# Optimization experiments

Measured on AMD Instinct MI355X. Metric: run time of the kernel, lower is better.

Reference implementation:

```python
import jax, jax.numpy as jnp
import numpy as np

EPS = 1e-12

def _l2norm(x):
    return x / jnp.maximum(jnp.linalg.norm(x, axis=-1, keepdims=True), EPS)

def setup_inputs() -> dict:
    key = jax.random.key(0)
    ks = jax.random.split(key, 11)
    B, L, HID, M = 64, 512, 768, 128
    R, P, T = 64, 8, 32
    return {
        "hidden_states": jax.random.normal(ks[0], (B, L, HID), dtype=jnp.float32),
        "ctx_mask": jax.random.randint(ks[1], (B, L), 0, 2, dtype=jnp.int32),
        "between_mask": jax.random.randint(ks[2], (B, L), 0, 2, dtype=jnp.int32),
        "subj_type_id": jax.random.randint(ks[3], (B,), 0, T, dtype=jnp.int32),
        "obj_type_id": jax.random.randint(ks[4], (B,), 0, T, dtype=jnp.int32),
        "subj_first": jax.random.randint(ks[5], (B,), 0, 2, dtype=jnp.int32),
        "proj_W": jax.random.normal(ks[6], (HID, M), dtype=jnp.float32) * 0.02,
        "label_probes": jax.random.normal(ks[7], (R, P, M), dtype=jnp.float32) * 0.02,
        "subj_type_W": jax.random.normal(ks[8], (T, M), dtype=jnp.float32) * 0.02,
        "obj_type_W": jax.random.normal(ks[9], (T, M), dtype=jnp.float32) * 0.02,
        "dir_W": jax.random.normal(ks[10], (2, M), dtype=jnp.float32) * 0.02,
    }

def reference(hidden_states, ctx_mask, between_mask, subj_type_id, obj_type_id,
              subj_first, proj_W, label_probes, subj_type_W, obj_type_W, dir_W):
    # Document token embeddings: project + L2 normalize. [B, L, M]
    D = _l2norm(hidden_states @ proj_W)

    between = between_mask.astype(bool)
    ctx = ctx_mask.astype(bool)
    has_between = jnp.any(between, axis=1)  # [B]
    evidence = jnp.where(has_between[:, None], between, ctx)  # [B, L]

    # Conditioned probes: [B, R, P, M]
    Q = (label_probes[None]
         + subj_type_W[subj_type_id][:, None, None]
         + obj_type_W[obj_type_id][:, None, None]
         + dir_W[subj_first][:, None, None])
    Q = _l2norm(Q)

    # MaxSim: [B, R, P, L]
    sim = jnp.einsum('brhm,blm->brhl', Q, D)
    sim = jnp.where(evidence[:, None, None, :], sim, -10000.0)
    mx = sim.max(axis=3)                        # [B, R, P]
    mx = jnp.where(mx > -1000.0, mx, 0.0)       # zero out fully-masked probes
    logits = mx.sum(axis=2)                     # [B, R]
    return logits
```

## Files before the change

### kernel.cpp

```cpp
#include <hip/hip_runtime.h>
#include <hip/hip_bf16.h>

typedef __attribute__((ext_vector_type(8))) __bf16 bf16x8;
typedef __attribute__((ext_vector_type(4))) float f32x4;

#define B_   64
#define L_   512
#define HID_ 768
#define M_   128
#define R_   64
#define P_   8

__device__ __forceinline__ int swz(int row, int k, int stride) {
    return row * stride + (k ^ ((row & 7) << 3));
}
__device__ __forceinline__ int swz4(int row, int k) {
    return row * 128 + (k ^ ((row & 15) << 3));
}

#define GLL16(gp, lp)                                                        \
    __builtin_amdgcn_global_load_lds(                                        \
        (const __attribute__((address_space(1))) void*)(gp),                 \
        (__attribute__((address_space(3))) void*)(lp), 16, 0, 0)

__device__ __forceinline__ bf16x8 cvt8(float4 f0, float4 f1) {
    bf16x8 v;
    v[0]=(__bf16)f0.x; v[1]=(__bf16)f0.y; v[2]=(__bf16)f0.z; v[3]=(__bf16)f0.w;
    v[4]=(__bf16)f1.x; v[5]=(__bf16)f1.y; v[6]=(__bf16)f1.z; v[7]=(__bf16)f1.w;
    return v;
}

__global__ __launch_bounds__(256) void k_wt(const float* __restrict__ W,
                                            __bf16* __restrict__ Wt) {
    int idx = blockIdx.x * 256 + threadIdx.x;
    int k = idx >> 7, n = idx & 127;
    int c = k >> 6, kk = k & 63;
    Wt[c * 8192 + n * 64 + (kk ^ ((n & 7) << 3))] = (__bf16)W[idx];
}

__global__ __launch_bounds__(512, 4) void k_proj(const float* __restrict__ hidden,
                                                 const __bf16* __restrict__ Wt,
                                                 __bf16* __restrict__ D) {
    __shared__ __align__(16) __bf16 Al[2][64 * 64];
    __shared__ __align__(16) __bf16 Bl[2][128 * 64];
    __shared__ float nbuf[2][64];
    const int t = threadIdx.x;
    const int lane = t & 63, w = t >> 6;
    const int rlo = lane & 15, g = lane >> 4;
    const int rb = w & 3, ch = w >> 2;
    const int row0 = blockIdx.x * 512 + blockIdx.y * 64;

    f32x4 acc[4] = {};

    const int ar = t >> 3;
    const int ac = (t & 7) * 8;
    const float* arow = hidden + (size_t)(row0 + ar) * HID_ + ac;

    GLL16(Wt + w * 1024 + lane * 8,       &Bl[0][w * 1024]);
    GLL16(Wt + w * 1024 + 512 + lane * 8, &Bl[0][w * 1024 + 512]);
    {
        float4 f0 = *(const float4*)(arow);
        float4 f1 = *(const float4*)(arow + 4);
        *(bf16x8*)&Al[0][swz(ar, ac, 64)] = cvt8(f0, f1);
    }
    __syncthreads();

    for (int ci = 0; ci < 12; ++ci) {
        const int cur = ci & 1;
        const bool pre = ci < 11;
        float4 f0, f1;
        if (pre) {
            const __bf16* wsrc = Wt + (ci + 1) * 8192 + w * 1024;
            GLL16(wsrc + lane * 8,       &Bl[cur ^ 1][w * 1024]);
            GLL16(wsrc + 512 + lane * 8, &Bl[cur ^ 1][w * 1024 + 512]);
            const float* src = arow + (ci + 1) * 64;
            f0 = *(const float4*)(src);
            f1 = *(const float4*)(src + 4);
        }
#pragma unroll
        for (int s = 0; s < 2; ++s) {
            int kk = s * 32 + g * 8;
            bf16x8 aF = *(const bf16x8*)&Al[cur][swz(rb * 16 + rlo, kk, 64)];
#pragma unroll
            for (int c = 0; c < 4; ++c) {
                bf16x8 bF = *(const bf16x8*)&Bl[cur][swz(ch * 64 + c * 16 + rlo, kk, 64)];
                acc[c] = __builtin_amdgcn_mfma_f32_16x16x32_bf16(aF, bF, acc[c], 0, 0, 0);
            }
        }
        if (pre) {
            *(bf16x8*)&Al[cur ^ 1][swz(ar, ac, 64)] = cvt8(f0, f1);
        }
        __syncthreads();
    }

    float ss[4] = {0.f, 0.f, 0.f, 0.f};
#pragma unroll
    for (int c = 0; c < 4; ++c)
#pragma unroll
        for (int r = 0; r < 4; ++r) ss[r] += acc[c][r] * acc[c][r];
#pragma unroll
    for (int r = 0; r < 4; ++r)
#pragma unroll
        for (int off = 1; off < 16; off <<= 1) ss[r] += __shfl_xor(ss[r], off);
    if (rlo == 0) {
#pragma unroll
        for (int r = 0; r < 4; ++r) nbuf[ch][rb * 16 + g * 4 + r] = ss[r];
    }
    __syncthreads();
    float sc[4];
#pragma unroll
    for (int r = 0; r < 4; ++r) {
        float tot = nbuf[0][rb * 16 + g * 4 + r] + nbuf[1][rb * 16 + g * 4 + r];
        sc[r] = 1.0f / fmaxf(sqrtf(tot), 1e-12f);
    }

    __bf16* Dst = (__bf16*)Al;
#pragma unroll
    for (int c = 0; c < 4; ++c)
#pragma unroll
        for (int r = 0; r < 4; ++r) {
            int row = rb * 16 + g * 4 + r;
            int col = ch * 64 + c * 16 + rlo;
            Dst[swz4(row, col)] = (__bf16)(acc[c][r] * sc[r]);
        }
    __syncthreads();
#pragma unroll
    for (int h = 0; h < 2; ++h) {
        int row = (t >> 4) + h * 32;
        int seg = t & 15;
        bf16x8 v = *(const bf16x8*)&Dst[row * 128 + seg * 8];
        *(bf16x8*)(D + (size_t)(row0 + row) * M_ + seg * 8) = v;
    }
}

__global__ __launch_bounds__(256) void k_sim(const float* __restrict__ lp,
                                             const float* __restrict__ sW,
                                             const float* __restrict__ oW,
                                             const float* __restrict__ dW,
                                             const int* __restrict__ st,
                                             const int* __restrict__ ot,
                                             const int* __restrict__ sf,
                                             const int* __restrict__ ctx,
                                             const int* __restrict__ btw,
                                             const __bf16* __restrict__ D,
                                             float* __restrict__ out) {
    __shared__ __align__(16) __bf16 Dl[2][128 * 128];
    __shared__ float evl[L_];
    __shared__ int anyf;
    const int t = threadIdx.x;
    const int lane = t & 63, w = t >> 6;
    const int rlo = lane & 15, g = lane >> 4;
    const int b = blockIdx.x, pt = blockIdx.y;

    const __bf16* Db = D + (size_t)b * L_ * M_;

#pragma unroll
    for (int q = 0; q < 8; ++q)
        GLL16(Db + q * 2048 + w * 512 + lane * 8, &Dl[0][q * 2048 + w * 512]);

    if (t == 0) anyf = 0;
    __syncthreads();
    int v0 = btw[b * L_ + t], v1 = btw[b * L_ + t + 256];
    int c0 = ctx[b * L_ + t], c1 = ctx[b * L_ + t + 256];
    if (v0 | v1) anyf = 1;
    __syncthreads();
    const int any = anyf;
    evl[t]       = (any ? v0 : c0) ? 1.0f : 0.0f;
    evl[t + 256] = (any ? v1 : c1) ? 1.0f : 0.0f;

    const int sb = st[b], ob = ot[b], db = sf[b];
    const float* sv = sW + sb * M_;
    const float* ov = oW + ob * M_;
    const float* dv = dW + db * M_;
    bf16x8 qF[2][4];
#pragma unroll
    for (int pt2 = 0; pt2 < 2; ++pt2) {
        const float* lpp = lp + (size_t)(pt * 128 + w * 32 + pt2 * 16 + rlo) * M_;
        float qv[32];
        float ssq = 0.f;
#pragma unroll
        for (int ks = 0; ks < 4; ++ks) {
#pragma unroll
            for (int h = 0; h < 2; ++h) {
                const int m0 = ks * 32 + g * 8 + h * 4;
                float4 a  = *(const float4*)(lpp + m0);
                float4 s4 = *(const float4*)(sv + m0);
                float4 o4 = *(const float4*)(ov + m0);
                float4 d4 = *(const float4*)(dv + m0);
                float x0 = a.x + s4.x + o4.x + d4.x;
                float x1 = a.y + s4.y + o4.y + d4.y;
                float x2 = a.z + s4.z + o4.z + d4.z;
                float x3 = a.w + s4.w + o4.w + d4.w;
                qv[ks * 8 + h * 4 + 0] = x0;
                qv[ks * 8 + h * 4 + 1] = x1;
                qv[ks * 8 + h * 4 + 2] = x2;
                qv[ks * 8 + h * 4 + 3] = x3;
                ssq += x0 * x0 + x1 * x1 + x2 * x2 + x3 * x3;
            }
        }
        ssq += __shfl_xor(ssq, 16);
        ssq += __shfl_xor(ssq, 32);
        const float scq = 1.0f / fmaxf(sqrtf(ssq), 1e-12f);
#pragma unroll
        for (int ks = 0; ks < 4; ++ks)
#pragma unroll
            for (int j = 0; j < 8; ++j)
                qF[pt2][ks][j] = (__bf16)(qv[ks * 8 + j] * scq);
    }

    __syncthreads();

    float vmax[2][4];
#pragma unroll
    for (int pt2 = 0; pt2 < 2; ++pt2)
#pragma unroll
        for (int r = 0; r < 4; ++r) vmax[pt2][r] = -1e30f;

    for (int tc = 0; tc < 4; ++tc) {
        const int cur = tc & 1;
        if (tc < 3) {
#pragma unroll
            for (int q = 0; q < 8; ++q)
                GLL16(Db + (tc + 1) * 16384 + q * 2048 + w * 512 + lane * 8,
                      &Dl[cur ^ 1][q * 2048 + w * 512]);
        }
#pragma unroll
        for (int tt = 0; tt < 8; ++tt) {
            f32x4 pacc[2] = {};
#pragma unroll
            for (int ks = 0; ks < 4; ++ks) {
                bf16x8 bF = *(const bf16x8*)&Dl[cur][swz4(tt * 16 + rlo, ks * 32 + g * 8)];
                pacc[0] = __builtin_amdgcn_mfma_f32_16x16x32_bf16(qF[0][ks], bF, pacc[0], 0, 0, 0);
                pacc[1] = __builtin_amdgcn_mfma_f32_16x16x32_bf16(qF[1][ks], bF, pacc[1], 0, 0, 0);
            }
            const float e = evl[tc * 128 + tt * 16 + rlo];
#pragma unroll
            for (int pt2 = 0; pt2 < 2; ++pt2)
#pragma unroll
                for (int r = 0; r < 4; ++r) {
                    float sv2 = (e > 0.5f) ? pacc[pt2][r] : -1e4f;
                    vmax[pt2][r] = fmaxf(vmax[pt2][r], sv2);
                }
        }
        __syncthreads();
    }

#pragma unroll
    for (int pt2 = 0; pt2 < 2; ++pt2)
#pragma unroll
        for (int r = 0; r < 4; ++r)
#pragma unroll
            for (int off = 1; off < 16; off <<= 1)
                vmax[pt2][r] = fmaxf(vmax[pt2][r], __shfl_xor(vmax[pt2][r], off));

#pragma unroll
    for (int pt2 = 0; pt2 < 2; ++pt2) {
        float psum = 0.f;
#pragma unroll
        for (int r = 0; r < 4; ++r)
            psum += (vmax[pt2][r] > -1000.0f) ? vmax[pt2][r] : 0.0f;
        float rtot = psum + __shfl_xor(psum, 16);
        if ((lane & 31) == 0) {
            int rr = pt * 16 + w * 4 + pt2 * 2 + (g >> 1);
            out[b * R_ + rr] = rtot;
        }
    }
}

extern "C" void kernel_launch(void* const* d_in, const int* in_sizes, int n_in,
                              void* d_out, int out_size, void* d_ws, size_t ws_size,
                              hipStream_t stream) {
    const float* hidden = (const float*)d_in[0];
    const int*   ctx    = (const int*)d_in[1];
    const int*   btw    = (const int*)d_in[2];
    const int*   st     = (const int*)d_in[3];
    const int*   ot     = (const int*)d_in[4];
    const int*   sf     = (const int*)d_in[5];
    const float* W      = (const float*)d_in[6];
    const float* lp     = (const float*)d_in[7];
    const float* sW     = (const float*)d_in[8];
    const float* oW     = (const float*)d_in[9];
    const float* dW     = (const float*)d_in[10];
    float* out = (float*)d_out;

    char* ws = (char*)d_ws;
    __bf16* Wt = (__bf16*)ws;
    __bf16* D  = (__bf16*)(ws + 196608);

    k_wt  <<<(HID_ * M_) / 256, 256, 0, stream>>>(W, Wt);
    k_proj<<<dim3(B_, 8), 512, 0, stream>>>(hidden, Wt, D);
    k_sim <<<dim3(B_, 4), 256, 0, stream>>>(lp, sW, oW, dW, st, ot, sf, ctx, btw, D, out);
}
```

Baseline: 44.08 us.

## Split sim kernel across L per wave, read D directly from global

The sim kernel no longer stages D tiles through double-buffered LDS. Each wave now reads its own 128-row slice of D directly from global memory using the swizzled layout. All four waves share the same 64 probes, so partial maxima are combined through a small shared array, and the grid doubles to 8 probe groups per batch. This removes the 64KB LDS footprint and the per-chunk barriers, which should raise occupancy, at the cost of uncoalesced global loads and redundant D reads across probe groups.

```diff
diff --git a/kernel.cpp b/kernel.cpp
--- a/kernel.cpp
+++ b/kernel.cpp
@@ -144,20 +144,14 @@
                                              const int* __restrict__ btw,
                                              const __bf16* __restrict__ D,
                                              float* __restrict__ out) {
-    __shared__ __align__(16) __bf16 Dl[2][128 * 128];
     __shared__ float evl[L_];
+    __shared__ float pmx[4][64];
     __shared__ int anyf;
     const int t = threadIdx.x;
     const int lane = t & 63, w = t >> 6;
     const int rlo = lane & 15, g = lane >> 4;
     const int b = blockIdx.x, pt = blockIdx.y;
 
-    const __bf16* Db = D + (size_t)b * L_ * M_;
-
-#pragma unroll
-    for (int q = 0; q < 8; ++q)
-        GLL16(Db + q * 2048 + w * 512 + lane * 8, &Dl[0][q * 2048 + w * 512]);
-
     if (t == 0) anyf = 0;
     __syncthreads();
     int v0 = btw[b * L_ + t], v1 = btw[b * L_ + t + 256];
@@ -172,10 +166,10 @@
     const float* sv = sW + sb * M_;
     const float* ov = oW + ob * M_;
     const float* dv = dW + db * M_;
-    bf16x8 qF[2][4];
-#pragma unroll
-    for (int pt2 = 0; pt2 < 2; ++pt2) {
-        const float* lpp = lp + (size_t)(pt * 128 + w * 32 + pt2 * 16 + rlo) * M_;
+    bf16x8 qF[4][4];
+#pragma unroll
+    for (int pt2 = 0; pt2 < 4; ++pt2) {
+        const float* lpp = lp + (size_t)(pt * 64 + pt2 * 16 + rlo) * M_;
         float qv[32];
         float ssq = 0.f;
 #pragma unroll
@@ -207,63 +201,62 @@
             for (int j = 0; j < 8; ++j)
                 qF[pt2][ks][j] = (__bf16)(qv[ks * 8 + j] * scq);
     }
-
-    __syncthreads();
-
-    float vmax[2][4];
-#pragma unroll
-    for (int pt2 = 0; pt2 < 2; ++pt2)
+    __syncthreads();
+
+    const __bf16* Db = D + (size_t)b * L_ * M_;
+    float vmax[4][4];
+#pragma unroll
+    for (int pt2 = 0; pt2 < 4; ++pt2)
 #pragma unroll
         for (int r = 0; r < 4; ++r) vmax[pt2][r] = -1e30f;
 
-    for (int tc = 0; tc < 4; ++tc) {
-        const int cur = tc & 1;
-        if (tc < 3) {
-#pragma unroll
-            for (int q = 0; q < 8; ++q)
-                GLL16(Db + (tc + 1) * 16384 + q * 2048 + w * 512 + lane * 8,
-                      &Dl[cur ^ 1][q * 2048 + w * 512]);
-        }
-#pragma unroll
-        for (int tt = 0; tt < 8; ++tt) {
-            f32x4 pacc[2] = {};
-#pragma unroll
-            for (int ks = 0; ks < 4; ++ks) {
-                bf16x8 bF = *(const bf16x8*)&Dl[cur][swz4(tt * 16 + rlo, ks * 32 + g * 8)];
-                pacc[0] = __builtin_amdgcn_mfma_f32_16x16x32_bf16(qF[0][ks], bF, pacc[0], 0, 0, 0);
-                pacc[1] = __builtin_amdgcn_mfma_f32_16x16x32_bf16(qF[1][ks], bF, pacc[1], 0, 0, 0);
+#pragma unroll 2
+    for (int i = 0; i < 8; ++i) {
+        const int tt = w * 8 + i;
+        const __bf16* rowp = Db + (size_t)(tt * 16 + rlo) * M_;
+        f32x4 pacc[4] = {};
+#pragma unroll
+        for (int ks = 0; ks < 4; ++ks) {
+            bf16x8 bF = *(const bf16x8*)(rowp + ((ks * 32 + g * 8) ^ (rlo << 3)));
+            pacc[0] = __builtin_amdgcn_mfma_f32_16x16x32_bf16(qF[0][ks], bF, pacc[0], 0, 0, 0);
+            pacc[1] = __builtin_amdgcn_mfma_f32_16x16x32_bf16(qF[1][ks], bF, pacc[1], 0, 0, 0);
+            pacc[2] = __builtin_amdgcn_mfma_f32_16x16x32_bf16(qF[2][ks], bF, pacc[2], 0, 0, 0);
+            pacc[3] = __builtin_amdgcn_mfma_f32_16x16x32_bf16(qF[3][ks], bF, pacc[3], 0, 0, 0);
+        }
+        const float e = evl[tt * 16 + rlo];
+#pragma unroll
+        for (int pt2 = 0; pt2 < 4; ++pt2)
+#pragma unroll
+            for (int r = 0; r < 4; ++r) {
+                float sv2 = (e > 0.5f) ? pacc[pt2][r] : -1e4f;
+                vmax[pt2][r] = fmaxf(vmax[pt2][r], sv2);
             }
-            const float e = evl[tc * 128 + tt * 16 + rlo];
-#pragma unroll
-            for (int pt2 = 0; pt2 < 2; ++pt2)
-#pragma unroll
-                for (int r = 0; r < 4; ++r) {
-                    float sv2 = (e > 0.5f) ? pacc[pt2][r] : -1e4f;
-                    vmax[pt2][r] = fmaxf(vmax[pt2][r], sv2);
-                }
-        }
-        __syncthreads();
-    }
-
-#pragma unroll
-    for (int pt2 = 0; pt2 < 2; ++pt2)
+    }
+
+#pragma unroll
+    for (int pt2 = 0; pt2 < 4; ++pt2)
 #pragma unroll
         for (int r = 0; r < 4; ++r)
 #pragma unroll
             for (int off = 1; off < 16; off <<= 1)
                 vmax[pt2][r] = fmaxf(vmax[pt2][r], __shfl_xor(vmax[pt2][r], off));
 
-#pragma unroll
-    for (int pt2 = 0; pt2 < 2; ++pt2) {
-        float psum = 0.f;
-#pragma unroll
-        for (int r = 0; r < 4; ++r)
-            psum += (vmax[pt2][r] > -1000.0f) ? vmax[pt2][r] : 0.0f;
-        float rtot = psum + __shfl_xor(psum, 16);
-        if ((lane & 31) == 0) {
-            int rr = pt * 16 + w * 4 + pt2 * 2 + (g >> 1);
-            out[b * R_ + rr] = rtot;
-        }
+    if (rlo == 0) {
+#pragma unroll
+        for (int pt2 = 0; pt2 < 4; ++pt2)
+#pragma unroll
+            for (int r = 0; r < 4; ++r)
+                pmx[w][pt2 * 16 + g * 4 + r] = vmax[pt2][r];
+    }
+    __syncthreads();
+
+    if (t < 64) {
+        float m = fmaxf(fmaxf(pmx[0][t], pmx[1][t]), fmaxf(pmx[2][t], pmx[3][t]));
+        m = (m > -1000.0f) ? m : 0.0f;
+        m += __shfl_xor(m, 1);
+        m += __shfl_xor(m, 2);
+        m += __shfl_xor(m, 4);
+        if ((t & 7) == 0) out[b * R_ + pt * 8 + (t >> 3)] = m;
     }
 }
 
@@ -289,5 +282,5 @@
 
     k_wt  <<<(HID_ * M_) / 256, 256, 0, stream>>>(W, Wt);
     k_proj<<<dim3(B_, 8), 512, 0, stream>>>(hidden, Wt, D);
-    k_sim <<<dim3(B_, 4), 256, 0, stream>>>(lp, sW, oW, dW, st, ot, sf, ctx, btw, D, out);
-}
+    k_sim <<<dim3(B_, 8), 256, 0, stream>>>(lp, sW, oW, dW, st, ot, sf, ctx, btw, D, out);
+}
```

Result: slower. 51.30 us (+16.4%).

## Stage fp32 activations directly into LDS via async loads, convert at fragment read

Applied to the files above, without the earlier changes.

The A-operand (hidden states) is now loaded asynchronously from global memory straight into LDS as fp32, using a swizzled layout, instead of going through registers with a bf16 conversion before the LDS store. The bf16 conversion moves to the point where MFMA fragments are read from LDS. Explicit vmcnt waits and raw s_barriers replace __syncthreads so the next chunk's loads overlap the current chunk's compute. The cost is doubled LDS for the A tile and conversion work repeated per fragment read, which may lower occupancy.

```diff
diff --git a/kernel.cpp b/kernel.cpp
--- a/kernel.cpp
+++ b/kernel.cpp
@@ -41,7 +41,7 @@
 __global__ __launch_bounds__(512, 4) void k_proj(const float* __restrict__ hidden,
                                                  const __bf16* __restrict__ Wt,
                                                  __bf16* __restrict__ D) {
-    __shared__ __align__(16) __bf16 Al[2][64 * 64];
+    __shared__ __align__(16) float  Alf[2][64 * 64];
     __shared__ __align__(16) __bf16 Bl[2][128 * 64];
     __shared__ float nbuf[2][64];
     const int t = threadIdx.x;
@@ -52,46 +52,61 @@
 
     f32x4 acc[4] = {};
 
-    const int ar = t >> 3;
-    const int ac = (t & 7) * 8;
-    const float* arow = hidden + (size_t)(row0 + ar) * HID_ + ac;
-
-    GLL16(Wt + w * 1024 + lane * 8,       &Bl[0][w * 1024]);
-    GLL16(Wt + w * 1024 + 512 + lane * 8, &Bl[0][w * 1024 + 512]);
-    {
-        float4 f0 = *(const float4*)(arow);
-        float4 f1 = *(const float4*)(arow + 4);
-        *(bf16x8*)&Al[0][swz(ar, ac, 64)] = cvt8(f0, f1);
-    }
-    __syncthreads();
+    const int sr0 = t >> 4;
+    const int scg = t & 15;
+    const float* hbase = hidden + (size_t)row0 * HID_;
+
+#define STAGE_A(ci_, buf_)                                                     \
+    {                                                                          \
+        _Pragma("unroll")                                                      \
+        for (int h = 0; h < 2; ++h) {                                          \
+            const int row = h * 32 + sr0;                                      \
+            const int cgs = scg ^ (row & 7);                                   \
+            GLL16(hbase + (size_t)row * HID_ + (ci_) * 64 + cgs * 4,           \
+                  &Alf[buf_][(h * 8 + w) * 256 + lane * 4]);                   \
+        }                                                                      \
+    }
+#define STAGE_B(ci_, buf_)                                                     \
+    {                                                                          \
+        const __bf16* wsrc = Wt + (ci_) * 8192 + w * 1024;                     \
+        GLL16(wsrc + lane * 8,       &Bl[buf_][w * 1024]);                     \
+        GLL16(wsrc + 512 + lane * 8, &Bl[buf_][w * 1024 + 512]);               \
+    }
+
+    STAGE_A(0, 0);
+    STAGE_B(0, 0);
 
     for (int ci = 0; ci < 12; ++ci) {
         const int cur = ci & 1;
-        const bool pre = ci < 11;
-        float4 f0, f1;
-        if (pre) {
-            const __bf16* wsrc = Wt + (ci + 1) * 8192 + w * 1024;
-            GLL16(wsrc + lane * 8,       &Bl[cur ^ 1][w * 1024]);
-            GLL16(wsrc + 512 + lane * 8, &Bl[cur ^ 1][w * 1024 + 512]);
-            const float* src = arow + (ci + 1) * 64;
-            f0 = *(const float4*)(src);
-            f1 = *(const float4*)(src + 4);
-        }
+        if (ci < 11) {
+            STAGE_A(ci + 1, cur ^ 1);
+            STAGE_B(ci + 1, cur ^ 1);
+            asm volatile("s_waitcnt vmcnt(4)" ::: "memory");
+        } else {
+            asm volatile("s_waitcnt vmcnt(0)" ::: "memory");
+        }
+        __builtin_amdgcn_sched_barrier(0);
+        __builtin_amdgcn_s_barrier();
+
 #pragma unroll
         for (int s = 0; s < 2; ++s) {
-            int kk = s * 32 + g * 8;
-            bf16x8 aF = *(const bf16x8*)&Al[cur][swz(rb * 16 + rlo, kk, 64)];
+            const int row = rb * 16 + rlo;
+            const int kkg = s * 8 + g * 2;
+            const int x = row & 7;
+            float4 a0 = *(const float4*)&Alf[cur][row * 64 + ((kkg ^ x) * 4)];
+            float4 a1 = *(const float4*)&Alf[cur][row * 64 + (((kkg + 1) ^ x) * 4)];
+            bf16x8 aF = cvt8(a0, a1);
+            const int kk = s * 32 + g * 8;
 #pragma unroll
             for (int c = 0; c < 4; ++c) {
                 bf16x8 bF = *(const bf16x8*)&Bl[cur][swz(ch * 64 + c * 16 + rlo, kk, 64)];
                 acc[c] = __builtin_amdgcn_mfma_f32_16x16x32_bf16(aF, bF, acc[c], 0, 0, 0);
             }
         }
-        if (pre) {
-            *(bf16x8*)&Al[cur ^ 1][swz(ar, ac, 64)] = cvt8(f0, f1);
-        }
-        __syncthreads();
-    }
+        __builtin_amdgcn_s_barrier();
+    }
+#undef STAGE_A
+#undef STAGE_B
 
     float ss[4] = {0.f, 0.f, 0.f, 0.f};
 #pragma unroll
@@ -114,7 +129,7 @@
         sc[r] = 1.0f / fmaxf(sqrtf(tot), 1e-12f);
     }
 
-    __bf16* Dst = (__bf16*)Al;
+    __bf16* Dst = (__bf16*)Alf;
 #pragma unroll
     for (int c = 0; c < 4; ++c)
 #pragma unroll
```

Result: faster. 42.07 us (median of 2 runs) (-4.6%).
